# Optimization experiments

Measured on AMD Instinct MI355X. Metric: run time of the kernel, lower is better.

Reference implementation:

```python
import jax, jax.numpy as jnp
import numpy as np

EPS = 1e-5       # BatchNorm eps (eval mode, running_mean=0, running_var=1)
TV_F = 1e-5      # FLAGS.tv_reg_factor
CT_F = 1e-4      # FLAGS.constrast_reg_factor


def conv2d(x, w):
    return jax.lax.conv_general_dilated(x, w, (1, 1), 'SAME',
                                        dimension_numbers=('NCHW', 'OIHW', 'NCHW'))


def bn(x, p):
    # eval-mode BN with running_mean=0, running_var=1: x/sqrt(1+eps)*gamma + beta
    g, b = p[0], p[1]
    s = g / jnp.sqrt(1.0 + EPS)
    return x * s[None, :, None, None] + b[None, :, None, None]


def two_conv(x, w1, p1, w2, p2):
    x = jax.nn.relu(bn(conv2d(x, w1), p1))
    return jax.nn.relu(bn(conv2d(x, w2), p2))


def setup_inputs() -> dict:
    key = jax.random.key(0)
    ks = jax.random.split(key, 20)
    B, T, C, H = 8, 16, 2048, 7
    f = lambda k, sh, s=0.02: jax.random.normal(k, sh, jnp.float32) * s
    bnp = lambda k, c: jnp.stack([1.0 + f(k, (c,), 0.05), jnp.zeros((c,), jnp.float32)])
    return {
        'input_x': jax.random.normal(ks[0], (B, C, T, H, H), jnp.float32),
        'mask_w1': f(ks[1], (1024, 2048, 3, 3)), 'mask_bn1': bnp(ks[2], 1024),
        'mask_w2': f(ks[3], (512, 1024, 3, 3)), 'mask_bn2': bnp(ks[4], 512),
        'mask_w3': f(ks[5], (1, 512, 3, 3)),
        'h0_w1': f(ks[6], (1024, 2048, 3, 3)), 'h0_bn1': bnp(ks[7], 1024),
        'h0_w2': f(ks[8], (512, 1024, 3, 3)), 'h0_bn2': bnp(ks[9], 512),
        'c0_w1': f(ks[10], (1024, 2048, 3, 3)), 'c0_bn1': bnp(ks[11], 1024),
        'c0_w2': f(ks[12], (512, 1024, 3, 3)), 'c0_bn2': bnp(ks[13], 512),
        'att_fw': f(ks[14], (1, 2048)), 'att_hw': f(ks[15], (1, 512)),
        'lstm_w': f(ks[16], (4 * 512, 2048 + 512, 3, 3)),
        'lstm_b': jnp.zeros((4 * 512,), jnp.float32),
        'fc_w': f(ks[17], (3, 512)), 'fc_b': jnp.zeros((3,), jnp.float32),
    }


def reference(input_x, mask_w1, mask_bn1, mask_w2, mask_bn2, mask_w3,
              h0_w1, h0_bn1, h0_w2, h0_bn2, c0_w1, c0_bn1, c0_w2, c0_bn2,
              att_fw, att_hw, lstm_w, lstm_b, fc_w, fc_b):
    B, C, T, H, W = input_x.shape
    # dropout_2d is identity in eval mode
    xr = jnp.transpose(input_x, (0, 2, 1, 3, 4)).reshape(B * T, C, H, W)

    # mask conv: 2048 -> 1024 -> 512 -> 1, sigmoid
    m = jax.nn.relu(bn(conv2d(xr, mask_w1), mask_bn1))
    m = jax.nn.relu(bn(conv2d(m, mask_w2), mask_bn2))
    mask = jax.nn.sigmoid(conv2d(m, mask_w3)).reshape(B, T, 1, H, W)

    tv_loss = TV_F * (jnp.sum(jnp.abs(mask[..., 1:] - mask[..., :-1]))
                      + jnp.sum(jnp.abs(mask[..., 1:, :] - mask[..., :-1, :])))
    mA = (mask > 0.5).astype(jnp.float32)
    mB = (mask < 0.5).astype(jnp.float32)
    contrast_loss = (-(mask * mA).mean(0).sum() * CT_F * 0.5
                     + (mask * mB).mean(0).sum() * CT_F * 0.5)

    mx = mask * xr.reshape(B, T, C, H, W)          # (B,T,2048,7,7)
    mean_x = mx.mean(1)                            # (B,2048,7,7)
    h = two_conv(mean_x, h0_w1, h0_bn1, h0_w2, h0_bn2)   # (B,512,7,7)
    c = two_conv(mean_x, c0_w1, c0_bn1, c0_w2, c0_bn2)

    # per-frame feature attention logits (constant across steps)
    att_fea = (mx.mean((3, 4)) @ att_fw.T)[..., 0]       # (B,T)

    def step(carry, _):
        h, c = carry
        att_h = h.mean((2, 3)) @ att_hw.T                # (B,1)
        w = jax.nn.softmax(att_fea + att_h, axis=1)      # (B,T)
        xt = jnp.einsum('btchw,bt->bchw', mx, w)         # attention-weighted frame
        z = conv2d(jnp.concatenate([xt, h], axis=1), lstm_w) + lstm_b[None, :, None, None]
        i, f, o, g = jnp.split(z, 4, axis=1)
        c2 = jax.nn.sigmoid(f) * c + jax.nn.sigmoid(i) * jnp.tanh(g)
        h2 = jax.nn.sigmoid(o) * jnp.tanh(c2)
        return (h2, c2), (h2.mean((2, 3)), w)

    (_, _), (outs, ws) = jax.lax.scan(step, (h, c), None, length=T)
    final_output = outs.mean(0) @ fc_w.T + fc_b          # (B, output_size)
    return final_output, ws[-1], mask, tv_loss, contrast_loss


if __name__ == '__main__':
    out = reference(**setup_inputs())
    print(out[0].shape, out[1].shape, out[2].shape)
```

## Files before the change

kernel.cpp:

```cpp
#include <hip/hip_runtime.h>
#include <cstdint>

typedef unsigned short u16;
typedef __bf16 bf16x8 __attribute__((ext_vector_type(8)));
typedef float f32x4 __attribute__((ext_vector_type(4)));

#define BNRS 0.9999950000374997f

__device__ __forceinline__ u16 f2bf(float f) {
  unsigned u = __float_as_uint(f);
  u += 0x7fffu + ((u >> 16) & 1u);
  return (u16)(u >> 16);
}
__device__ __forceinline__ float bf2f(u16 h) {
  return __uint_as_float(((unsigned)h) << 16);
}

__device__ __forceinline__ void glds16(const u16* g, u16* l) {
  __builtin_amdgcn_global_load_lds(
      (const __attribute__((address_space(1))) void*)g,
      (__attribute__((address_space(3))) void*)l, 16, 0, 0);
}

#define OFF_XN     0ull
#define OFF_M1     42467328ull
#define OFF_M2     63700992ull
#define SZ_M2      10616832ull
#define OFF_MEANX  63700992ull
#define OFF_XTN    66355200ull
#define OFF_TH1    69009408ull
#define OFF_TC1    70336512ull
#define OFF_HN     71663616ull
#define OFF_CST    72327168ull
#define OFF_ZXACC  74317824ull
#define OFF_ATH1   77529088ull
#define OFF_ATC1   79134720ull
#define OFF_ATH2   80740352ull
#define OFF_ATC2   81543168ull
#define OFF_FEA    82345984ull
#define OFF_W      82346496ull
#define OFF_OUTS   82347008ull
#define Z0_END     82378752ull
#define OFF_WA     82378752ull
#define OFF_WB     120127488ull
#define OFF_MX     129564672ull
#define OFF_M1ACC  129564672ull
#define OFF_M2ACC  155254784ull
#define SZ_MACC    38535168ull
#define OFF_LSTMW  82378752ull
#define OFF_ZPART  176750592ull
#define ARENA_END  202440704ull

#define CF_BN    1
#define CF_RELU  2
#define CF_ATOM  4
#define CF_OUTF  8
#define CF_OUTB 16
#define CF_ZOFF 32

__global__ __launch_bounds__(256)
void k_conv(const u16* __restrict__ Xin, const u16* __restrict__ Wt,
            float* __restrict__ outF, u16* __restrict__ outB,
            float* __restrict__ atomF,
            const float* __restrict__ gamma, const float* __restrict__ beta,
            int M, int Cin, int log2Cin, int ldb, int Cout, int kChunk, int flags)
{
  __shared__ u16 As[128*32];
  __shared__ u16 Bs[128*32];
  const int tid = threadIdx.x;
  const int m0 = blockIdx.x*128, n0 = blockIdx.y*128;
  const int row0 = tid >> 2;
  const int c8 = (((tid & 3) ^ (row0 & 3) ^ ((row0 >> 2) & 3))) * 8;

  long long Abase[2], Bbase[2];
  #pragma unroll
  for (int r = 0; r < 2; ++r) {
    int m = m0 + row0 + r*64; if (m > M-1) m = M-1;
    int img = m / 49, p = m % 49, y = p / 7, xx = p % 7;
    Abase[r] = (long long)(img*81 + y*9 + xx) * Cin + c8;
    Bbase[r] = (long long)(n0 + row0 + r*64) * ldb + c8;
  }
  const long long tapStride = (long long)Cout * ldb;
  const int lane = tid & 63, wave = tid >> 6;
  const int l16 = lane & 15, quad = lane >> 4;
  const int wm = wave & 1, wn = wave >> 1;
  const int fsl = (quad ^ (l16 & 3) ^ ((l16 >> 2) & 3)) * 8;
  const u16* Afr = As + (wm*64 + l16)*32 + fsl;
  const u16* Bfr = Bs + (wn*64 + l16)*32 + fsl;
  u16* ldsA0 = As + wave*512;
  u16* ldsA1 = As + 2048 + wave*512;
  u16* ldsB0 = Bs + wave*512;
  u16* ldsB1 = Bs + 2048 + wave*512;

  f32x4 acc[4][4];
  #pragma unroll
  for (int i=0;i<4;i++)
    #pragma unroll
    for (int j=0;j<4;j++)
      #pragma unroll
      for (int r=0;r<4;r++) acc[i][j][r] = 0.f;

  const int kStart = blockIdx.z * kChunk, kEnd = kStart + kChunk;
  for (int kk = kStart; kk < kEnd; kk += 32) {
    int tap = kk >> log2Cin;
    int kc  = kk & (Cin - 1);
    int ty  = tap / 3;
    int tapAdd = (ty*6 + tap) << log2Cin;
    const u16* ga0 = Xin + Abase[0] + tapAdd + kc;
    const u16* ga1 = Xin + Abase[1] + tapAdd + kc;
    const u16* wp  = Wt + (long long)tap * tapStride + kc;
    const u16* gb0 = wp + Bbase[0];
    const u16* gb1 = wp + Bbase[1];
    __syncthreads();
    glds16(ga0, ldsA0);
    glds16(ga1, ldsA1);
    glds16(gb0, ldsB0);
    glds16(gb1, ldsB1);
    __syncthreads();
    bf16x8 av[4], bv[4];
    #pragma unroll
    for (int i=0;i<4;i++) av[i] = *(const bf16x8*)(Afr + i*16*32);
    #pragma unroll
    for (int j=0;j<4;j++) bv[j] = *(const bf16x8*)(Bfr + j*16*32);
    #pragma unroll
    for (int i=0;i<4;i++)
      #pragma unroll
      for (int j=0;j<4;j++)
        acc[i][j] = __builtin_amdgcn_mfma_f32_16x16x32_bf16(av[i], bv[j], acc[i][j], 0, 0, 0);
  }

  float* outFz = outF;
  if (flags & CF_ZOFF) outFz = outF + (long long)blockIdx.z * M * Cout;
  #pragma unroll
  for (int i=0;i<4;i++) {
    #pragma unroll
    for (int r=0;r<4;r++) {
      int m = m0 + wm*64 + i*16 + quad*4 + r;
      if (m >= M) continue;
      int img = m / 49, p = m % 49;
      int pp = (p/7 + 1)*9 + (p%7) + 1;
      #pragma unroll
      for (int j=0;j<4;j++) {
        int n = n0 + wn*64 + j*16 + l16;
        float v = acc[i][j][r];
        if (flags & CF_BN)   v = v * (gamma[n]*BNRS) + beta[n];
        if (flags & CF_RELU) v = fmaxf(v, 0.f);
        if (flags & CF_ATOM) atomicAdd(atomF + (long long)m*Cout + n, v);
        if (flags & CF_OUTF) outFz[(long long)m*Cout + n] = v;
        if (flags & CF_OUTB) outB[((long long)img*81 + pp)*Cout + n] = f2bf(v);
      }
    }
  }
}

__global__ void k_wtrans(const float* __restrict__ W, u16* __restrict__ Wt, int total) {
  int idx = blockIdx.x*256 + threadIdx.x;
  if (idx >= total) return;
  const float* src = W + (long long)idx*9;
  #pragma unroll
  for (int tap=0; tap<9; ++tap)
    Wt[(long long)tap*total + idx] = f2bf(src[tap]);
}

__global__ void k_transpose(const float* __restrict__ x, u16* __restrict__ Xn) {
  int idx = blockIdx.x*256 + threadIdx.x;
  int p = idx % 49; int r = idx / 49; int c8 = (r & 255)*8; int b = r >> 8;
  if (b >= 8) return;
  int pp = (p/7 + 1)*9 + (p%7) + 1;
  for (int t=0; t<16; ++t) {
    u16 o[8];
    #pragma unroll
    for (int j=0;j<8;j++)
      o[j] = f2bf(x[((long long)(b*2048 + c8 + j)*16 + t)*49 + p]);
    *(uint4*)&Xn[((long long)(b*16+t)*81 + pp)*2048 + c8] = *(uint4*)o;
  }
}

__global__ void k_mask3(const u16* __restrict__ M2b, const float* __restrict__ w3,
                        float* __restrict__ maskOut) {
  int img = blockIdx.x / 49, p = blockIdx.x % 49;
  int y = p/7, xx = p%7;
  int lane = threadIdx.x;
  float s = 0.f;
  for (int k = lane; k < 4608; k += 64) {
    int tap = k >> 9, c = k & 511;
    int ty = tap/3, tx = tap - ty*3;
    int pp = (y+ty)*9 + xx + tx;
    s += bf2f(M2b[((long long)img*81 + pp)*512 + c]) * w3[c*9 + tap];
  }
  #pragma unroll
  for (int off=32; off>0; off>>=1) s += __shfl_down(s, off, 64);
  if (lane == 0) maskOut[blockIdx.x] = 1.f/(1.f + expf(-s));
}

__global__ void k_losses(const float* __restrict__ mk, float* __restrict__ dout) {
  __shared__ float s1[256], s2[256];
  int tid = threadIdx.x;
  float tv = 0.f, ct = 0.f;
  for (int i = tid; i < 128*7*6; i += 256) {
    int img = i / 42, r = i % 42, y = r / 6, xx = r % 6;
    int base = img*49 + y*7 + xx;
    tv += fabsf(mk[base+1] - mk[base]);
  }
  for (int i = tid; i < 128*6*7; i += 256) {
    int img = i / 42, r = i % 42, y = r / 7, xx = r % 7;
    int base = img*49 + y*7 + xx;
    tv += fabsf(mk[base+7] - mk[base]);
  }
  for (int i = tid; i < 6272; i += 256) {
    float v = mk[i];
    ct += (v < 0.5f ? v : 0.f) - (v > 0.5f ? v : 0.f);
  }
  s1[tid] = tv; s2[tid] = ct; __syncthreads();
  for (int off=128; off>0; off>>=1) {
    if (tid < off) { s1[tid]+=s1[tid+off]; s2[tid]+=s2[tid+off]; }
    __syncthreads();
  }
  if (tid==0) { dout[6424] = 1e-5f * s1[0]; dout[6425] = (1e-4f*0.5f/8.f) * s2[0]; }
}

__global__ void k_mx(const float* __restrict__ x, const float* __restrict__ mk,
                     u16* __restrict__ mxn, u16* __restrict__ meanx) {
  int idx = blockIdx.x*256 + threadIdx.x;
  int p = idx % 49; int r = idx / 49; int c8 = (r & 255)*8; int b = r >> 8;
  if (b >= 8) return;
  int pp = (p/7+1)*9 + (p%7) + 1;
  float macc[8] = {0,0,0,0,0,0,0,0};
  for (int t=0;t<16;++t) {
    float mval = mk[(b*16+t)*49 + p];
    u16 o[8];
    #pragma unroll
    for (int j=0;j<8;j++) {
      float v = x[((long long)(b*2048 + c8 + j)*16 + t)*49 + p] * mval;
      o[j] = f2bf(v); macc[j] += v;
    }
    *(uint4*)&mxn[((long long)(b*16+t)*81 + pp)*2048 + c8] = *(uint4*)o;
  }
  u16 o2[8];
  #pragma unroll
  for (int j=0;j<8;j++) o2[j] = f2bf(macc[j] * (1.f/16.f));
  *(uint4*)&meanx[((long long)b*81 + pp)*2048 + c8] = *(uint4*)o2;
}

__global__ void k_att(const u16* __restrict__ mxn, const float* __restrict__ fw,
                      float* __restrict__ fea) {
  __shared__ float red[256];
  int img = blockIdx.x, tid = threadIdx.x;
  const u16* base = mxn + (long long)img*81*2048;
  float s = 0.f;
  for (int k = tid; k < 49*2048; k += 256) {
    int p = k >> 11, c = k & 2047;
    int pp = (p/7+1)*9 + (p%7) + 1;
    s += bf2f(base[(long long)pp*2048 + c]) * fw[c];
  }
  red[tid] = s; __syncthreads();
  for (int off=128; off>0; off>>=1) { if (tid<off) red[tid]+=red[tid+off]; __syncthreads(); }
  if (tid==0) fea[img] = red[0] * (1.f/49.f);
}

__global__ void k_softmax(const float* __restrict__ fea, float* __restrict__ w,
                          float* __restrict__ doutW) {
  int b = threadIdx.x;
  if (b >= 8) return;
  float mx = -1e30f;
  for (int t=0;t<16;t++) mx = fmaxf(mx, fea[b*16+t]);
  float e[16], s = 0.f;
  for (int t=0;t<16;t++) { e[t] = expf(fea[b*16+t]-mx); s += e[t]; }
  float inv = 1.f/s;
  for (int t=0;t<16;t++) { float v = e[t]*inv; w[b*16+t] = v; doutW[b*16+t] = v; }
}

__global__ void k_xt(const u16* __restrict__ mxn, const float* __restrict__ w,
                     u16* __restrict__ xtn) {
  int idx = blockIdx.x*256 + threadIdx.x;
  int c8 = (idx & 255)*8; int r = idx >> 8; int p = r % 49; int b = r / 49;
  if (b >= 8) return;
  int pp = (p/7+1)*9 + (p%7)+1;
  float a[8] = {0,0,0,0,0,0,0,0};
  for (int t=0;t<16;t++) {
    float wt = w[b*16+t];
    uint4 raw = *(const uint4*)&mxn[((long long)(b*16+t)*81 + pp)*2048 + c8];
    const u16* h = (const u16*)&raw;
    #pragma unroll
    for (int j=0;j<8;j++) a[j] += wt * bf2f(h[j]);
  }
  u16 o[8];
  #pragma unroll
  for (int j=0;j<8;j++) o[j] = f2bf(a[j]);
  *(uint4*)&xtn[((long long)b*81+pp)*2048 + c8] = *(uint4*)o;
}

__global__ void k_finalize(const float* __restrict__ acc, const float* __restrict__ bn,
                           u16* __restrict__ outB, float* __restrict__ outF,
                           int C, int nImg) {
  int idx = blockIdx.x*256 + threadIdx.x;
  int total = nImg*81*C;
  if (idx >= total) return;
  int c = idx % C; int r = idx / C; int pp = r % 81; int img = r / 81;
  int py = pp/9, px = pp%9;
  bool inter = (py>=1 && py<=7 && px>=1 && px<=7);
  float v = 0.f;
  int m = img*49 + (py-1)*7 + (px-1);
  if (inter) {
    v = acc[(long long)m*C + c];
    v = v*(bn[c]*BNRS) + bn[C+c];
    v = fmaxf(v, 0.f);
  }
  if (outB) outB[idx] = f2bf(v);
  if (outF && inter) outF[(long long)m*C + c] = v;
}

__global__ void k_gate(const float* __restrict__ zx, const float* __restrict__ zp,
                       const float* __restrict__ lb, float* __restrict__ cst,
                       u16* __restrict__ hn, float* __restrict__ outs) {
  int idx = blockIdx.x*256 + threadIdx.x;
  if (idx >= 392*512) return;
  int c = idx & 511; int m = idx >> 9;
  int b = m / 49, p = m % 49;
  int pp = (p/7+1)*9 + (p%7)+1;
  const float* zr = zx + (long long)m*2048;
  float zi = zr[c]        + lb[c];
  float zf = zr[c+512]    + lb[c+512];
  float zo = zr[c+1024]   + lb[c+1024];
  float zg = zr[c+1536]   + lb[c+1536];
  #pragma unroll
  for (int s=0;s<8;s++) {
    const float* q = zp + ((long long)s*392 + m)*2048;
    zi += q[c]; zf += q[c+512]; zo += q[c+1024]; zg += q[c+1536];
  }
  float si = 1.f/(1.f+expf(-zi));
  float sf = 1.f/(1.f+expf(-zf));
  float so = 1.f/(1.f+expf(-zo));
  float cn = sf*cst[idx] + si*tanhf(zg);
  float h  = so*tanhf(cn);
  cst[idx] = cn;
  hn[((long long)b*81 + pp)*512 + c] = f2bf(h);
  atomicAdd(outs + b*512 + c, h*(1.f/784.f));
}

__global__ void k_fc(const float* __restrict__ outs, const float* __restrict__ fcw,
                     const float* __restrict__ fcb, float* __restrict__ dout) {
  int t = threadIdx.x;
  if (t >= 24) return;
  int b = t / 3, j = t % 3;
  float s = fcb[j];
  for (int c=0;c<512;c++) s += outs[b*512+c]*fcw[j*512+c];
  dout[b*3+j] = s;
}

extern "C" void kernel_launch(void* const* d_in, const int* in_sizes, int n_in,
                              void* d_out, int out_size, void* d_ws, size_t ws_size,
                              hipStream_t stream) {
  (void)in_sizes; (void)n_in; (void)out_size;
  const float* x        = (const float*)d_in[0];
  const float* mask_w1  = (const float*)d_in[1];
  const float* mask_bn1 = (const float*)d_in[2];
  const float* mask_w2  = (const float*)d_in[3];
  const float* mask_bn2 = (const float*)d_in[4];
  const float* mask_w3  = (const float*)d_in[5];
  const float* h0_w1    = (const float*)d_in[6];
  const float* h0_bn1   = (const float*)d_in[7];
  const float* h0_w2    = (const float*)d_in[8];
  const float* h0_bn2   = (const float*)d_in[9];
  const float* c0_w1    = (const float*)d_in[10];
  const float* c0_bn1   = (const float*)d_in[11];
  const float* c0_w2    = (const float*)d_in[12];
  const float* c0_bn2   = (const float*)d_in[13];
  const float* att_fw   = (const float*)d_in[14];
  const float* lstm_w   = (const float*)d_in[16];
  const float* lstm_b   = (const float*)d_in[17];
  const float* fc_w     = (const float*)d_in[18];
  const float* fc_b     = (const float*)d_in[19];
  float* dout = (float*)d_out;
  char* ws = (char*)d_ws;
  if (ws_size < ARENA_END) return;

  u16* XN    = (u16*)(ws + OFF_XN);
  u16* M1b   = (u16*)(ws + OFF_M1);
  u16* M2b   = (u16*)(ws + OFF_M2);
  u16* MEANX = (u16*)(ws + OFF_MEANX);
  u16* XTN   = (u16*)(ws + OFF_XTN);
  u16* TH1   = (u16*)(ws + OFF_TH1);
  u16* TC1   = (u16*)(ws + OFF_TC1);
  u16* HN    = (u16*)(ws + OFF_HN);
  float* CST   = (float*)(ws + OFF_CST);
  float* ZXACC = (float*)(ws + OFF_ZXACC);
  float* ATH1  = (float*)(ws + OFF_ATH1);
  float* ATC1  = (float*)(ws + OFF_ATC1);
  float* ATH2  = (float*)(ws + OFF_ATH2);
  float* ATC2  = (float*)(ws + OFF_ATC2);
  float* FEA   = (float*)(ws + OFF_FEA);
  float* Wbuf  = (float*)(ws + OFF_W);
  float* OUTS  = (float*)(ws + OFF_OUTS);
  u16* WA    = (u16*)(ws + OFF_WA);
  u16* WB    = (u16*)(ws + OFF_WB);
  u16* MX    = (u16*)(ws + OFF_MX);
  u16* LSTMW = (u16*)(ws + OFF_LSTMW);
  float* ZPART = (float*)(ws + OFF_ZPART);
  float* M1ACC = (float*)(ws + OFF_M1ACC);
  float* M2ACC = (float*)(ws + OFF_M2ACC);

  hipMemsetAsync(ws, 0, (size_t)Z0_END, stream);
  hipMemsetAsync(ws + OFF_M1ACC, 0, (size_t)SZ_MACC, stream);

  k_wtrans<<<8192, 256, 0, stream>>>(mask_w1, WA, 1024*2048);
  k_wtrans<<<2048, 256, 0, stream>>>(mask_w2, WB, 512*1024);
  k_transpose<<<392, 256, 0, stream>>>(x, XN);
  k_conv<<<dim3(49,8,4),256,0,stream>>>(XN, WA, nullptr, nullptr, M1ACC,
      nullptr, nullptr, 6272, 2048, 11, 2048, 1024, 4608, CF_ATOM);
  k_finalize<<<41472, 256, 0, stream>>>(M1ACC, mask_bn1, M1b, nullptr, 1024, 128);
  k_conv<<<dim3(49,4,4),256,0,stream>>>(M1b, WB, nullptr, nullptr, M2ACC,
      nullptr, nullptr, 6272, 1024, 10, 1024, 512, 2304, CF_ATOM);
  k_finalize<<<20736, 256, 0, stream>>>(M2ACC, mask_bn2, M2b, nullptr, 512, 128);
  k_mask3<<<6272, 64, 0, stream>>>(M2b, mask_w3, dout+152);
  k_losses<<<1, 256, 0, stream>>>(dout+152, dout);

  hipMemsetAsync(ws + OFF_M2, 0, (size_t)SZ_M2, stream);
  k_mx<<<392, 256, 0, stream>>>(x, dout+152, MX, MEANX);
  k_att<<<128, 256, 0, stream>>>(MX, att_fw, FEA);
  k_softmax<<<1, 64, 0, stream>>>(FEA, Wbuf, dout+24);
  k_xt<<<392, 256, 0, stream>>>(MX, Wbuf, XTN);

  k_wtrans<<<8192, 256, 0, stream>>>(h0_w1, WA, 1024*2048);
  k_wtrans<<<2048, 256, 0, stream>>>(h0_w2, WB, 512*1024);
  k_conv<<<dim3(4,8,16),256,0,stream>>>(MEANX, WA, nullptr, nullptr, ATH1,
      nullptr, nullptr, 392, 2048, 11, 2048, 1024, 1152, CF_ATOM);
  k_finalize<<<2592, 256, 0, stream>>>(ATH1, h0_bn1, TH1, nullptr, 1024, 8);
  k_conv<<<dim3(4,4,16),256,0,stream>>>(TH1, WB, nullptr, nullptr, ATH2,
      nullptr, nullptr, 392, 1024, 10, 1024, 512, 576, CF_ATOM);
  k_finalize<<<1296, 256, 0, stream>>>(ATH2, h0_bn2, HN, nullptr, 512, 8);

  k_wtrans<<<8192, 256, 0, stream>>>(c0_w1, WA, 1024*2048);
  k_wtrans<<<2048, 256, 0, stream>>>(c0_w2, WB, 512*1024);
  k_conv<<<dim3(4,8,16),256,0,stream>>>(MEANX, WA, nullptr, nullptr, ATC1,
      nullptr, nullptr, 392, 2048, 11, 2048, 1024, 1152, CF_ATOM);
  k_finalize<<<2592, 256, 0, stream>>>(ATC1, c0_bn1, TC1, nullptr, 1024, 8);
  k_conv<<<dim3(4,4,16),256,0,stream>>>(TC1, WB, nullptr, nullptr, ATC2,
      nullptr, nullptr, 392, 1024, 10, 1024, 512, 576, CF_ATOM);
  k_finalize<<<1296, 256, 0, stream>>>(ATC2, c0_bn2, nullptr, CST, 512, 8);

  k_wtrans<<<20480, 256, 0, stream>>>(lstm_w, LSTMW, 2048*2560);
  k_conv<<<dim3(4,16,16),256,0,stream>>>(XTN, LSTMW, nullptr, nullptr, ZXACC,
      nullptr, nullptr, 392, 2048, 11, 2560, 2048, 1152, CF_ATOM);
  for (int step = 0; step < 16; ++step) {
    k_conv<<<dim3(4,16,8),256,0,stream>>>(HN, LSTMW+2048, ZPART, nullptr, nullptr,
        nullptr, nullptr, 392, 512, 9, 2560, 2048, 576, CF_OUTF|CF_ZOFF);
    k_gate<<<784, 256, 0, stream>>>(ZXACC, ZPART, lstm_b, CST, HN, OUTS);
  }
  k_fc<<<1, 64, 0, stream>>>(OUTS, fc_w, fc_b, dout);
}
```

Baseline: 2.297 ms.

## Double-buffer LDS tiles in conv GEMM and remap blocks across XCDs

The implicit-GEMM conv kernel now uses two LDS buffers, so the global-to-LDS loads for the next K slice are issued while MFMAs run on the current one. This removes the load-then-wait stall on every K step. Block indices are also remapped so consecutive panels of the N/split-K grid land on the same XCD, which should improve L2 reuse of weights and activations. The loop now assumes kChunk is a multiple of 64, and LDS use doubles, which may reduce occupancy.

```diff
diff --git a/kernel.cpp b/kernel.cpp
--- a/kernel.cpp
+++ b/kernel.cpp
@@ -65,10 +65,22 @@
             const float* __restrict__ gamma, const float* __restrict__ beta,
             int M, int Cin, int log2Cin, int ldb, int Cout, int kChunk, int flags)
 {
-  __shared__ u16 As[128*32];
-  __shared__ u16 Bs[128*32];
+  __shared__ u16 As0[4096], As1[4096], Bs0[4096], Bs1[4096];
   const int tid = threadIdx.x;
-  const int m0 = blockIdx.x*128, n0 = blockIdx.y*128;
+
+  int bx = blockIdx.x, by = blockIdx.y, bz = blockIdx.z;
+  {
+    const int gx = gridDim.x, gy = gridDim.y;
+    const int P = gy * gridDim.z;
+    if ((P & 7) == 0) {
+      int flat = bx + gx * (by + gy * bz);
+      int xcd = flat & 7, local = flat >> 3, ppx = P >> 3;
+      int x = local / ppx, pl = local - x * ppx;
+      int panel = xcd * ppx + pl;
+      bx = x; by = panel % gy; bz = panel / gy;
+    }
+  }
+  const int m0 = bx*128, n0 = by*128;
   const int row0 = tid >> 2;
   const int c8 = (((tid & 3) ^ (row0 & 3) ^ ((row0 >> 2) & 3))) * 8;
 
@@ -85,12 +97,7 @@
   const int l16 = lane & 15, quad = lane >> 4;
   const int wm = wave & 1, wn = wave >> 1;
   const int fsl = (quad ^ (l16 & 3) ^ ((l16 >> 2) & 3)) * 8;
-  const u16* Afr = As + (wm*64 + l16)*32 + fsl;
-  const u16* Bfr = Bs + (wn*64 + l16)*32 + fsl;
-  u16* ldsA0 = As + wave*512;
-  u16* ldsA1 = As + 2048 + wave*512;
-  u16* ldsB0 = Bs + wave*512;
-  u16* ldsB1 = Bs + 2048 + wave*512;
+  const int stg = wave*512;
 
   f32x4 acc[4][4];
   #pragma unroll
@@ -100,37 +107,50 @@
       #pragma unroll
       for (int r=0;r<4;r++) acc[i][j][r] = 0.f;
 
-  const int kStart = blockIdx.z * kChunk, kEnd = kStart + kChunk;
-  for (int kk = kStart; kk < kEnd; kk += 32) {
-    int tap = kk >> log2Cin;
-    int kc  = kk & (Cin - 1);
-    int ty  = tap / 3;
-    int tapAdd = (ty*6 + tap) << log2Cin;
-    const u16* ga0 = Xin + Abase[0] + tapAdd + kc;
-    const u16* ga1 = Xin + Abase[1] + tapAdd + kc;
-    const u16* wp  = Wt + (long long)tap * tapStride + kc;
-    const u16* gb0 = wp + Bbase[0];
-    const u16* gb1 = wp + Bbase[1];
+  const int kStart = bz * kChunk, kEnd = kStart + kChunk;
+
+#define STAGE(KK, AB, BB) do {                                            \
+    int tap_ = (KK) >> log2Cin;                                           \
+    int kc_  = (KK) & (Cin - 1);                                          \
+    int ty_  = tap_ / 3;                                                  \
+    long long off_ = ((long long)(ty_*6 + tap_) << log2Cin) + kc_;        \
+    glds16(Xin + Abase[0] + off_, (AB) + stg);                            \
+    glds16(Xin + Abase[1] + off_, (AB) + 2048 + stg);                     \
+    const u16* wp_ = Wt + (long long)tap_ * tapStride + kc_;              \
+    glds16(wp_ + Bbase[0], (BB) + stg);                                   \
+    glds16(wp_ + Bbase[1], (BB) + 2048 + stg);                            \
+  } while(0)
+
+#define COMPUTE(AB, BB) do {                                              \
+    const u16* Af_ = (AB) + (wm*64 + l16)*32 + fsl;                       \
+    const u16* Bf_ = (BB) + (wn*64 + l16)*32 + fsl;                       \
+    bf16x8 av[4], bv[4];                                                  \
+    _Pragma("unroll")                                                     \
+    for (int i=0;i<4;i++) av[i] = *(const bf16x8*)(Af_ + i*512);          \
+    _Pragma("unroll")                                                     \
+    for (int j=0;j<4;j++) bv[j] = *(const bf16x8*)(Bf_ + j*512);          \
+    _Pragma("unroll")                                                     \
+    for (int i=0;i<4;i++)                                                 \
+      _Pragma("unroll")                                                   \
+      for (int j=0;j<4;j++)                                               \
+        acc[i][j] = __builtin_amdgcn_mfma_f32_16x16x32_bf16(av[i], bv[j], acc[i][j], 0, 0, 0); \
+  } while(0)
+
+  STAGE(kStart, As0, Bs0);
+  __syncthreads();
+  for (int kk = kStart; kk < kEnd; kk += 64) {
+    STAGE(kk + 32, As1, Bs1);
+    COMPUTE(As0, Bs0);
     __syncthreads();
-    glds16(ga0, ldsA0);
-    glds16(ga1, ldsA1);
-    glds16(gb0, ldsB0);
-    glds16(gb1, ldsB1);
+    if (kk + 64 < kEnd) STAGE(kk + 64, As0, Bs0);
+    COMPUTE(As1, Bs1);
     __syncthreads();
-    bf16x8 av[4], bv[4];
-    #pragma unroll
-    for (int i=0;i<4;i++) av[i] = *(const bf16x8*)(Afr + i*16*32);
-    #pragma unroll
-    for (int j=0;j<4;j++) bv[j] = *(const bf16x8*)(Bfr + j*16*32);
-    #pragma unroll
-    for (int i=0;i<4;i++)
-      #pragma unroll
-      for (int j=0;j<4;j++)
-        acc[i][j] = __builtin_amdgcn_mfma_f32_16x16x32_bf16(av[i], bv[j], acc[i][j], 0, 0, 0);
-  }
+  }
+#undef STAGE
+#undef COMPUTE
 
   float* outFz = outF;
-  if (flags & CF_ZOFF) outFz = outF + (long long)blockIdx.z * M * Cout;
+  if (flags & CF_ZOFF) outFz = outF + (long long)bz * M * Cout;
   #pragma unroll
   for (int i=0;i<4;i++) {
     #pragma unroll
```

Measured after the change: 2.072 ms. 9.8% less time.
